# Kernel optimization log

Measured on AMD Instinct MI355X. Metric: run time of the kernel, lower is better.

## Reference

```python
import jax, jax.numpy as jnp
from jax import lax
import numpy as np

C = 16          # channel_n
HID = 128       # hidden_size
FIRE_RATE = 0.5
STEP_SIZE = 1.0
B, H, W = 16, 192, 192


def setup_inputs() -> dict:
    key = jax.random.key(0)
    ks = jax.random.split(key, 8)
    return {
        "x": jax.random.uniform(ks[0], (B, C, H, W), dtype=jnp.float32),
        "w1": jax.random.normal(ks[1], (HID, 3 * C), dtype=jnp.float32) * 0.1,
        "b1": jax.random.normal(ks[2], (HID,), dtype=jnp.float32) * 0.1,
        "w2": jax.random.normal(ks[3], (HID, HID), dtype=jnp.float32) * 0.1,
        "b2": jax.random.normal(ks[4], (HID,), dtype=jnp.float32) * 0.1,
        "w3": jax.random.normal(ks[5], (C, HID), dtype=jnp.float32) * 0.1,
        "b3": jax.random.normal(ks[6], (C,), dtype=jnp.float32) * 0.1,
        "fire_noise": jax.random.uniform(ks[7], (B, 1, H, W), dtype=jnp.float32),
    }


def _living_mask(x):
    # max_pool2d(alpha, 3, stride=1, pad=1) > 0.1 on alpha channel 3
    alpha = x[:, 3:4, :, :]
    m = lax.reduce_window(alpha, -jnp.inf, lax.max,
                          (1, 1, 3, 3), (1, 1, 1, 1), 'SAME')
    return m > 0.1


def _depthwise(x, k2d):
    # k2d: (3,3); depthwise conv over all C channels with same kernel
    kern = jnp.tile(k2d[None, None, :, :], (x.shape[1], 1, 1, 1))  # (C,1,3,3)
    return lax.conv_general_dilated(
        x, kern, window_strides=(1, 1), padding='SAME',
        feature_group_count=x.shape[1],
        dimension_numbers=('NCHW', 'OIHW', 'NCHW'))


def _relu6(x):
    return jnp.clip(x, 0.0, 6.0)


def reference(x, w1, b1, w2, b2, w3, b3, fire_noise):
    pre_life = _living_mask(x)

    # perceive: identity + sobel-x + sobel-y (angle = 0)
    sx = jnp.asarray(np.outer([1, 2, 1], [-1, 0, 1]) / 8.0, dtype=x.dtype)
    sy = sx.T
    y = jnp.concatenate([x, _depthwise(x, sx), _depthwise(x, sy)], axis=1)  # (B,3C,H,W)

    # pointwise MLP (1x1 convs) with ReLU6
    h = _relu6(jnp.einsum('bchw,oc->bohw', y, w1) + b1[None, :, None, None])
    h = _relu6(jnp.einsum('bchw,oc->bohw', h, w2) + b2[None, :, None, None])
    dx = (jnp.einsum('bchw,oc->bohw', h, w3) + b3[None, :, None, None]) * STEP_SIZE

    update_mask = (fire_noise <= FIRE_RATE).astype(x.dtype)  # (B,1,H,W)
    x_new = x + dx * update_mask

    post_life = _living_mask(x_new)
    life_mask = (pre_life & post_life).astype(x.dtype)
    return x_new * life_mask
```

## Files before the change

kernel.cpp:

```cpp
#include <hip/hip_runtime.h>

typedef _Float16 half8  __attribute__((ext_vector_type(8)));
typedef _Float16 half4  __attribute__((ext_vector_type(4)));
typedef float    f32x4  __attribute__((ext_vector_type(4)));
typedef float    f32x16 __attribute__((ext_vector_type(16)));

#define WH_HALVES      26624
#define ALPHA_BYTE_OFF 53248

#define NBLOCKS  512
#define NTILES   2304

__global__ __launch_bounds__(256) void prep_weights(
    const float* __restrict__ w1, const float* __restrict__ w2,
    const float* __restrict__ w3, _Float16* __restrict__ wh)
{
    int i = blockIdx.x * 256 + threadIdx.x;
    if (i >= WH_HALVES) return;
    int f = i >> 9, rem = i & 511;
    int l = rem >> 3, j = rem & 7;
    int l31 = l & 31, hi = l >> 5;
    _Float16 v;
    if (f < 12) {
        int nb = f / 3, kb = f % 3;
        v = (_Float16)w1[(nb * 32 + l31) * 48 + kb * 16 + hi * 8 + j];
    } else if (f < 44) {
        int ff = f - 12, nb = ff >> 3, kb = ff & 7;
        v = (_Float16)w2[(nb * 32 + l31) * 128 + kb * 16 + hi * 8 + j];
    } else {
        int kb = f - 44;
        v = (l31 < 16) ? (_Float16)w3[l31 * 128 + kb * 16 + hi * 8 + j] : (_Float16)0.f;
    }
    wh[i] = v;
}

#define HALO_UNITS 1360

__device__ __forceinline__ void halo_loads(const float* __restrict__ x,
                                           int bb, int h0, int w0, int tid,
                                           float pfv[3][4])
{
#pragma unroll
    for (int k = 0; k < 3; ++k) {
        int u = tid + k * 512;
        bool valid = (u < HALO_UNITS);
        int uu = valid ? u : 0;
        int row = uu / 136, rem = uu % 136;
        int col = rem >> 2, cq = rem & 3;
        int hh = h0 - 1 + row, ww = w0 - 1 + col;
        bool inb = valid && hh >= 0 && hh < 192 && ww >= 0 && ww < 192;
#pragma unroll
        for (int cc = 0; cc < 4; ++cc)
            pfv[k][cc] = inb ? x[(((size_t)bb * 16 + cq * 4 + cc) * 192 + hh) * 192 + ww] : 0.f;
    }
}

__device__ __forceinline__ void halo_store(_Float16* __restrict__ dst, int tid,
                                           const float pfv[3][4])
{
#pragma unroll
    for (int k = 0; k < 3; ++k) {
        int u = tid + k * 512;
        if (u < HALO_UNITS) {
            int row = u / 136, rem = u % 136;
            int col = rem >> 2, cq = rem & 3;
            half4 hv;
#pragma unroll
            for (int cc = 0; cc < 4; ++cc) hv[cc] = (_Float16)pfv[k][cc];
            *(half4*)&dst[(row * 34 + col) * 16 + cq * 4] = hv;
        }
    }
}

__device__ __forceinline__ void make_frags(const f32x16 acc, half8* fa, half8* fb)
{
    unsigned P[8];
#pragma unroll
    for (int w = 0; w < 8; ++w) {
        float lo = __builtin_amdgcn_fmed3f(acc[2 * w    ], 0.f, 6.f);
        float hh = __builtin_amdgcn_fmed3f(acc[2 * w + 1], 0.f, 6.f);
        P[w] = __builtin_bit_cast(unsigned, __builtin_amdgcn_cvt_pkrtz(lo, hh));
    }
    asm volatile("v_permlane32_swap_b32 %0, %1" : "+v"(P[0]), "+v"(P[2]));
    asm volatile("v_permlane32_swap_b32 %0, %1" : "+v"(P[1]), "+v"(P[3]));
    asm volatile("v_permlane32_swap_b32 %0, %1" : "+v"(P[4]), "+v"(P[6]));
    asm volatile("v_permlane32_swap_b32 %0, %1" : "+v"(P[5]), "+v"(P[7]));
    union { unsigned u[4]; half8 h; } A, B;
    A.u[0] = P[0]; A.u[1] = P[1]; A.u[2] = P[2]; A.u[3] = P[3];
    B.u[0] = P[4]; B.u[1] = P[5]; B.u[2] = P[6]; B.u[3] = P[7];
    *fa = A.h; *fb = B.h;
}

__global__ __launch_bounds__(512, 4) void ca_main(
    const float* __restrict__ x,
    const float* __restrict__ b1g, const float* __restrict__ b2g,
    const float* __restrict__ b3g,
    const float* __restrict__ fire,
    const _Float16* __restrict__ wh,
    float* __restrict__ out,
    float* __restrict__ alpha_out)
{
    __shared__ __align__(16) struct {
        _Float16 w[WH_HALVES];
        _Float16 halo[2][10][34][16];
        __align__(64) float b1d[4][2][16];
        __align__(64) float b2d[4][2][16];
        __align__(64) float b3d[2][16];
    } s;

    const int tid  = threadIdx.x;
    const int lane = tid & 63;
    const int wave = tid >> 6;
    const int l31 = lane & 31, hi = lane >> 5;

    {
        const uint4* src = (const uint4*)wh;
        uint4* dst = (uint4*)&s.w[0];
        for (int i = tid; i < 3328; i += 512) dst[i] = src[i];
    }
    if (tid < 128) {
        int o = tid, nb = o >> 5, ol = o & 31;
        int r = (ol & 3) + 4 * (ol >> 3), hd = (ol >> 2) & 1;
        s.b1d[nb][hd][r] = b1g[o];
        s.b2d[nb][hd][r] = b2g[o];
    }
    if (tid < 32) {
        int hd = tid >> 4, r = tid & 15;
        s.b3d[hd][r] = (r < 8) ? b3g[(r & 3) + 8 * (r >> 2) + 4 * hd] : 0.f;
    }
    {
        int t = blockIdx.x;
        int bb = t / 144, rem = t % 144;
        int h0 = (rem / 6) * 8, w0 = (rem % 6) * 32;
        float pfv[3][4];
        halo_loads(x, bb, h0, w0, tid, pfv);
        halo_store(&s.halo[0][0][0][0], tid, pfv);
    }
    __syncthreads();

    const half8* wf = (const half8*)s.w;
    const int prow = wave, pcol = l31;
    const f32x16 b3reg = *(const f32x16*)&s.b3d[hi][0];

    for (int it = 0; ; ++it) {
        int t = blockIdx.x + it * NBLOCKS;
        if (t >= NTILES) break;
        int bb = t / 144, rem = t % 144;
        int h0 = (rem / 6) * 8, w0 = (rem % 6) * 32;
        const _Float16* hal = &s.halo[it & 1][0][0][0];

        float pfv[3][4];
        int tn = t + NBLOCKS;
        const bool have_next = (tn < NTILES);
        if (have_next) {
            int bbn = tn / 144, remn = tn % 144;
            halo_loads(x, bbn, (remn / 6) * 8, (remn % 6) * 32, tid, pfv);
        }
        const float fn = fire[(((size_t)bb) * 192 + h0 + prow) * 192 + w0 + pcol];

        half8 bs0, bs1, bs2;
        {
            half8 tp[3][3];
#pragma unroll
            for (int dr = 0; dr < 3; ++dr)
#pragma unroll
                for (int dc = 0; dc < 3; ++dc)
                    tp[dr][dc] = *(const half8*)&hal[((prow + dr) * 34 + pcol + dc) * 16 + hi * 8];
            half8 gxa = (tp[0][2] - tp[0][0]) + (tp[2][2] - tp[2][0]);
            half8 gxb = (tp[1][2] - tp[1][0]);
            half8 gx  = gxa + gxb + gxb;
            half8 gya = (tp[2][0] - tp[0][0]) + (tp[2][2] - tp[0][2]);
            half8 gyb = (tp[2][1] - tp[0][1]);
            half8 gy  = gya + gyb + gyb;
            const _Float16 e = (_Float16)0.125f;
            bs0 = tp[1][1];
            bs1 = gx * e;
            bs2 = gy * e;
        }

        half8 l2b[8];
#pragma unroll
        for (int nb = 0; nb < 4; ++nb) {
            f32x16 acc = *(const f32x16*)&s.b1d[nb][hi][0];
            acc = __builtin_amdgcn_mfma_f32_32x32x16_f16(wf[(nb * 3 + 0) * 64 + lane], bs0, acc, 0, 0, 0);
            acc = __builtin_amdgcn_mfma_f32_32x32x16_f16(wf[(nb * 3 + 1) * 64 + lane], bs1, acc, 0, 0, 0);
            acc = __builtin_amdgcn_mfma_f32_32x32x16_f16(wf[(nb * 3 + 2) * 64 + lane], bs2, acc, 0, 0, 0);
            make_frags(acc, &l2b[2 * nb], &l2b[2 * nb + 1]);
        }

        half8 l3b[8];
#pragma unroll
        for (int nb = 0; nb < 4; ++nb) {
            f32x16 acc = *(const f32x16*)&s.b2d[nb][hi][0];
#pragma unroll
            for (int kb = 0; kb < 8; ++kb)
                acc = __builtin_amdgcn_mfma_f32_32x32x16_f16(wf[(12 + nb * 8 + kb) * 64 + lane], l2b[kb], acc, 0, 0, 0);
            make_frags(acc, &l3b[2 * nb], &l3b[2 * nb + 1]);
        }

        f32x16 acc3 = b3reg;
#pragma unroll
        for (int kb = 0; kb < 8; ++kb)
            acc3 = __builtin_amdgcn_mfma_f32_32x32x16_f16(wf[(44 + kb) * 64 + lane], l3b[kb], acc3, 0, 0, 0);

        {
            half4 xq0 = *(const half4*)&hal[((1 + prow) * 34 + 1 + pcol) * 16 + hi * 4];
            half4 xq1 = *(const half4*)&hal[((1 + prow) * 34 + 1 + pcol) * 16 + 8 + hi * 4];
            const bool upd = (fn <= 0.5f);
            size_t obase = (((size_t)bb * 16) * 192 + h0 + prow) * 192 + w0 + pcol;
#pragma unroll
            for (int r = 0; r < 8; ++r) {
                int c = (r & 3) + 8 * (r >> 2) + 4 * hi;
                float xc = (float)((r < 4) ? xq0[r & 3] : xq1[r & 3]);
                float xn = xc + (upd ? acc3[r] : 0.f);
                out[obase + (size_t)c * 36864] = xn;
                if (hi == 0 && r == 3)
                    alpha_out[(((size_t)bb) * 192 + h0 + prow) * 192 + w0 + pcol] = xn;
            }
        }

        if (have_next)
            halo_store(&s.halo[(it + 1) & 1][0][0][0], tid, pfv);
        __syncthreads();
    }
}

__global__ __launch_bounds__(256) void ca_mask(
    const float* __restrict__ x,
    const float* __restrict__ alpha_new,
    float* __restrict__ out)
{
    int pix = blockIdx.x * 256 + threadIdx.x;
    int ww = pix % 192; int t = pix / 192;
    int hh = t % 192;   int bb = t / 192;
    float pre = -1e30f, post = -1e30f;
#pragma unroll
    for (int di = -1; di <= 1; ++di) {
        int nh = hh + di;
        if (nh < 0 || nh >= 192) continue;
#pragma unroll
        for (int dj = -1; dj <= 1; ++dj) {
            int nw = ww + dj;
            if (nw < 0 || nw >= 192) continue;
            pre  = fmaxf(pre,  x[(((size_t)bb * 16 + 3) * 192 + nh) * 192 + nw]);
            post = fmaxf(post, alpha_new[(((size_t)bb) * 192 + nh) * 192 + nw]);
        }
    }
    bool alive = (pre > 0.1f) && (post > 0.1f);
    if (alive) return;
#pragma unroll
    for (int c = 0; c < 16; ++c) {
        out[(((size_t)bb * 16 + c) * 192 + hh) * 192 + ww] = 0.f;
    }
}

extern "C" void kernel_launch(void* const* d_in, const int* in_sizes, int n_in,
                              void* d_out, int out_size, void* d_ws, size_t ws_size,
                              hipStream_t stream) {
    const float* x    = (const float*)d_in[0];
    const float* w1   = (const float*)d_in[1];
    const float* b1   = (const float*)d_in[2];
    const float* w2   = (const float*)d_in[3];
    const float* b2   = (const float*)d_in[4];
    const float* w3   = (const float*)d_in[5];
    const float* b3   = (const float*)d_in[6];
    const float* fire = (const float*)d_in[7];
    float* out = (float*)d_out;

    _Float16* wh     = (_Float16*)d_ws;
    float* alpha_new = (float*)((char*)d_ws + ALPHA_BYTE_OFF);

    prep_weights<<<104, 256, 0, stream>>>(w1, w2, w3, wh);
    ca_main<<<NBLOCKS, 512, 0, stream>>>(x, b1, b2, b3, fire, wh, out, alpha_new);
    ca_mask<<<2304, 256, 0, stream>>>(x, alpha_new, out);
}
```

Baseline: 65.66 us.

## Use atomic work-stealing tile scheduler and raise wave priority around MFMA chain

Replaces the static round-robin tile assignment (blockIdx + it*NBLOCKS) with a dynamic scheduler: a global counter, reset in prep_weights, is advanced with atomicAdd, and a three-slot ring in shared memory holds the current, next and next-after tile indices, so prefetch still works. The aim is to balance load when the 2304 tiles do not divide evenly across 512 persistent blocks or when blocks progress at different rates. It also wraps the MFMA layers in s_setprio(1)/s_setprio(0) to favour waves that are issuing matrix work. In exchange it adds atomic traffic per tile and an extra barrier at startup.

```diff
diff --git a/kernel.cpp b/kernel.cpp
--- a/kernel.cpp
+++ b/kernel.cpp
@@ -7,14 +7,17 @@
 
 #define WH_HALVES      26624
 #define ALPHA_BYTE_OFF 53248
+#define CNT_BYTE_OFF   (53248 + 16*192*192*4)
 
 #define NBLOCKS  512
 #define NTILES   2304
 
 __global__ __launch_bounds__(256) void prep_weights(
     const float* __restrict__ w1, const float* __restrict__ w2,
-    const float* __restrict__ w3, _Float16* __restrict__ wh)
-{
+    const float* __restrict__ w3, _Float16* __restrict__ wh,
+    unsigned* __restrict__ cnt)
+{
+    if (blockIdx.x == 0 && threadIdx.x == 0) *cnt = 0u;
     int i = blockIdx.x * 256 + threadIdx.x;
     if (i >= WH_HALVES) return;
     int f = i >> 9, rem = i & 511;
@@ -98,7 +101,8 @@
     const float* __restrict__ fire,
     const _Float16* __restrict__ wh,
     float* __restrict__ out,
-    float* __restrict__ alpha_out)
+    float* __restrict__ alpha_out,
+    unsigned* __restrict__ cnt)
 {
     __shared__ __align__(16) struct {
         _Float16 w[WH_HALVES];
@@ -106,6 +110,7 @@
         __align__(64) float b1d[4][2][16];
         __align__(64) float b2d[4][2][16];
         __align__(64) float b3d[2][16];
+        int tslot[3];
     } s;
 
     const int tid  = threadIdx.x;
@@ -113,6 +118,10 @@
     const int wave = tid >> 6;
     const int l31 = lane & 31, hi = lane >> 5;
 
+    if (tid == 0) {
+        s.tslot[0] = (int)atomicAdd(cnt, 1u);
+        s.tslot[1] = (int)atomicAdd(cnt, 1u);
+    }
     {
         const uint4* src = (const uint4*)wh;
         uint4* dst = (uint4*)&s.w[0];
@@ -128,29 +137,32 @@
         int hd = tid >> 4, r = tid & 15;
         s.b3d[hd][r] = (r < 8) ? b3g[(r & 3) + 8 * (r >> 2) + 4 * hd] : 0.f;
     }
+    __syncthreads();
+
     {
-        int t = blockIdx.x;
+        int t0 = s.tslot[0];
+        if (t0 < NTILES) {
+            int bb = t0 / 144, rem = t0 % 144;
+            float pfv[3][4];
+            halo_loads(x, bb, (rem / 6) * 8, (rem % 6) * 32, tid, pfv);
+            halo_store(&s.halo[0][0][0][0], tid, pfv);
+        }
+    }
+    __syncthreads();
+
+    const half8* wf = (const half8*)&s.w[0];
+    const int prow = wave, pcol = l31;
+    const f32x16 b3reg = *(const f32x16*)&s.b3d[hi][0];
+
+    for (int p = 0; ; ++p) {
+        const int t = s.tslot[p % 3];
+        if (t >= NTILES) break;
+        const int tn = s.tslot[(p + 1) % 3];
         int bb = t / 144, rem = t % 144;
         int h0 = (rem / 6) * 8, w0 = (rem % 6) * 32;
+        const _Float16* hal = &s.halo[p & 1][0][0][0];
+
         float pfv[3][4];
-        halo_loads(x, bb, h0, w0, tid, pfv);
-        halo_store(&s.halo[0][0][0][0], tid, pfv);
-    }
-    __syncthreads();
-
-    const half8* wf = (const half8*)s.w;
-    const int prow = wave, pcol = l31;
-    const f32x16 b3reg = *(const f32x16*)&s.b3d[hi][0];
-
-    for (int it = 0; ; ++it) {
-        int t = blockIdx.x + it * NBLOCKS;
-        if (t >= NTILES) break;
-        int bb = t / 144, rem = t % 144;
-        int h0 = (rem / 6) * 8, w0 = (rem % 6) * 32;
-        const _Float16* hal = &s.halo[it & 1][0][0][0];
-
-        float pfv[3][4];
-        int tn = t + NBLOCKS;
         const bool have_next = (tn < NTILES);
         if (have_next) {
             int bbn = tn / 144, remn = tn % 144;
@@ -178,6 +190,8 @@
             bs2 = gy * e;
         }
 
+        __builtin_amdgcn_s_setprio(1);
+
         half8 l2b[8];
 #pragma unroll
         for (int nb = 0; nb < 4; ++nb) {
@@ -202,6 +216,8 @@
 #pragma unroll
         for (int kb = 0; kb < 8; ++kb)
             acc3 = __builtin_amdgcn_mfma_f32_32x32x16_f16(wf[(44 + kb) * 64 + lane], l3b[kb], acc3, 0, 0, 0);
+
+        __builtin_amdgcn_s_setprio(0);
 
         {
             half4 xq0 = *(const half4*)&hal[((1 + prow) * 34 + 1 + pcol) * 16 + hi * 4];
@@ -219,8 +235,9 @@
             }
         }
 
+        if (tid == 0) s.tslot[(p + 2) % 3] = (int)atomicAdd(cnt, 1u);
         if (have_next)
-            halo_store(&s.halo[(it + 1) & 1][0][0][0], tid, pfv);
+            halo_store(&s.halo[(p + 1) & 1][0][0][0], tid, pfv);
         __syncthreads();
     }
 }
@@ -269,8 +286,9 @@
 
     _Float16* wh     = (_Float16*)d_ws;
     float* alpha_new = (float*)((char*)d_ws + ALPHA_BYTE_OFF);
-
-    prep_weights<<<104, 256, 0, stream>>>(w1, w2, w3, wh);
-    ca_main<<<NBLOCKS, 512, 0, stream>>>(x, b1, b2, b3, fire, wh, out, alpha_new);
+    unsigned* cnt    = (unsigned*)((char*)d_ws + CNT_BYTE_OFF);
+
+    prep_weights<<<104, 256, 0, stream>>>(w1, w2, w3, wh, cnt);
+    ca_main<<<NBLOCKS, 512, 0, stream>>>(x, b1, b2, b3, fire, wh, out, alpha_new, cnt);
     ca_mask<<<2304, 256, 0, stream>>>(x, alpha_new, out);
 }
```

Result: slower. 76.49 us (+16.5%).
